# Optimization experiments

Measured on AMD Instinct MI355X. Metric: run time of the kernel, lower is better.

Reference implementation:

```python
import jax, jax.numpy as jnp
import numpy as np

EMBED = 1024

def setup_inputs() -> dict:
    key = jax.random.key(0)
    ks = jax.random.split(key, 7)
    s = 1.0 / np.sqrt(EMBED)
    x = jax.random.normal(ks[0], (8, 2048, EMBED), dtype=jnp.float32)
    Wq = jax.random.normal(ks[1], (EMBED, EMBED), dtype=jnp.float32) * s
    bq = jax.random.normal(ks[2], (EMBED,), dtype=jnp.float32) * s
    Wk = jax.random.normal(ks[3], (EMBED, EMBED), dtype=jnp.float32) * s
    bk = jax.random.normal(ks[4], (EMBED,), dtype=jnp.float32) * s
    Wv = jax.random.normal(ks[5], (EMBED, EMBED), dtype=jnp.float32) * s
    bv = jax.random.normal(ks[6], (EMBED,), dtype=jnp.float32) * s
    return {"x": x, "Wq": Wq, "bq": bq, "Wk": Wk, "bk": bk, "Wv": Wv, "bv": bv}

def reference(x, Wq, bq, Wk, bk, Wv, bv):
    # Linear layers: y = x @ W^T + b (torch convention)
    Q = jnp.einsum('bse,fe->bsf', x, Wq) + bq
    K = jnp.einsum('bse,fe->bsf', x, Wk) + bk
    V = jnp.einsum('bse,fe->bsf', x, Wv) + bv
    scale = 1.0 / jnp.sqrt(jnp.asarray(x.shape[-1], x.dtype))
    scores = jnp.einsum('bqe,bke->bqk', Q, K) * scale  # [B, S, S]
    weights = jax.nn.softmax(scores, axis=-1)
    # dropout is identity in eval mode (deterministic reference)
    return jnp.einsum('bqk,bke->bqe', weights, V)
```

## Files before the change

### kernel.cpp

```cpp
#include <hip/hip_runtime.h>

typedef __bf16 bf16x8 __attribute__((ext_vector_type(8)));
typedef float f32x4 __attribute__((ext_vector_type(4)));

__device__ __forceinline__ unsigned short f2bf(float f) {
  unsigned int u = __builtin_bit_cast(unsigned int, f);
  u += 0x7fffu + ((u >> 16) & 1u);
  return (unsigned short)(u >> 16);
}

__device__ __forceinline__ void async16(const void* g, void* l) {
  __builtin_amdgcn_global_load_lds(
      (const __attribute__((address_space(1))) unsigned int*)g,
      (__attribute__((address_space(3))) unsigned int*)l, 16, 0, 0);
}

#define MFMA(a, b, c) __builtin_amdgcn_mfma_f32_16x16x32_bf16((a), (b), (c), 0, 0, 0)

__global__ __launch_bounds__(256) void pack_bf16(const float* __restrict__ src,
                                                 unsigned short* __restrict__ dst,
                                                 long n) {
  long i = ((long)blockIdx.x * blockDim.x + threadIdx.x) * 4;
  long stride = (long)gridDim.x * blockDim.x * 4;
  for (; i < n; i += stride) {
    float4 v = *(const float4*)(src + i);
    ushort4 o;
    o.x = f2bf(v.x); o.y = f2bf(v.y); o.z = f2bf(v.z); o.w = f2bf(v.w);
    *(ushort4*)(dst + i) = o;
  }
}

template <int EPI>
__global__ __launch_bounds__(512, 1) void gemm256(
    const unsigned short* __restrict__ A, long sAz,
    const unsigned short* __restrict__ B, long sBz,
    int lda, int ldb, int nt,
    float* __restrict__ Cf, long sCz, int ldc, float scale,
    unsigned short* __restrict__ Cq, long sQz, int ldq,
    const float* __restrict__ bq, const float* __restrict__ bk,
    const float* __restrict__ bv,
    float* __restrict__ psum, const float* __restrict__ rsum) {
  extern __shared__ __align__(16) char smem[];
  const int tid = threadIdx.x;
  const int l = tid & 63;
  const int w = tid >> 6;
  const int wm = w >> 2, wn = w & 3;
  int bm = blockIdx.x;
  if ((gridDim.x & 7) == 0) {
    int cpx = gridDim.x >> 3;
    bm = (bm & 7) * cpx + (bm >> 3);
  }
  const int bn = blockIdx.y, bz = blockIdx.z;
  const unsigned short* Ab = A + (long)bz * sAz + (long)bm * 256 * lda;
  const unsigned short* Bb = B + (long)bz * sBz + (long)bn * 256 * ldb;

  const int r0 = tid >> 3;
  const int sch = (tid & 7) ^ (r0 & 7);
  const int l15 = l & 15;
  const int kof = (l >> 4) << 3;

  const int aslot = wm * 16384;
  const int bslot = 32768 + (wn >> 1) * 16384;
  const int brow0 = (wn & 1) * 64;

  int aof[8][2], bof[4][2];
#pragma unroll
  for (int fr = 0; fr < 8; ++fr)
#pragma unroll
    for (int ks = 0; ks < 2; ++ks) {
      int rins = fr * 16 + l15;
      int byte = aslot + rins * 128 + (ks * 32 + kof) * 2;
      aof[fr][ks] = byte ^ ((rins & 7) << 4);
    }
#pragma unroll
  for (int fc = 0; fc < 4; ++fc)
#pragma unroll
    for (int ks = 0; ks < 2; ++ks) {
      int rins = brow0 + fc * 16 + l15;
      int byte = bslot + rins * 128 + (ks * 32 + kof) * 2;
      bof[fc][ks] = byte ^ ((rins & 7) << 4);
    }

  const unsigned short* pa0 = Ab + (long)r0 * lda + sch * 8;
  const unsigned short* pa1 = pa0 + (long)64 * lda;
  const unsigned short* pa2 = pa0 + (long)128 * lda;
  const unsigned short* pa3 = pa0 + (long)192 * lda;
  const unsigned short* pb0 = Bb + (long)r0 * ldb + sch * 8;
  const unsigned short* pb1 = pb0 + (long)64 * ldb;
  const unsigned short* pb2 = pb0 + (long)128 * ldb;
  const unsigned short* pb3 = pb0 + (long)192 * ldb;

  char* sdst = smem + (tid << 4);

  f32x4 acc[8][4] = {};
  bf16x8 bfr[4][2];

#define LDA_FRAG(dst, bb, fr, ks) \
  dst = *(const bf16x8*)(smem + (aof[fr][ks] + (bb)));
#define LDB_FRAG(dst, bb, fc, ks) \
  dst = *(const bf16x8*)(smem + (bof[fc][ks] + (bb)));

  async16(pb0, sdst + 32768);         async16(pb1, sdst + 40960);
  async16(pb2, sdst + 49152);         async16(pb3, sdst + 57344);
  async16(pa0, sdst + 0);             async16(pa1, sdst + 8192);
  async16(pa2, sdst + 16384);         async16(pa3, sdst + 24576);
  async16(pb0 + 64, sdst + 98304);    async16(pb1 + 64, sdst + 106496);
  async16(pb2 + 64, sdst + 114688);   async16(pb3 + 64, sdst + 122880);
  asm volatile("s_waitcnt vmcnt(4)" ::: "memory");
  __builtin_amdgcn_s_barrier();
  pa0 += 64; pa1 += 64; pa2 += 64; pa3 += 64;
  pb0 += 128; pb1 += 128; pb2 += 128; pb3 += 128;

  for (int t = 0; t < nt; ++t) {
    const int buf = (t & 1) << 16;
    const int nbuf = buf ^ 65536;

    bf16x8 a00, a01, a10, a11;

    LDA_FRAG(a00, buf, 0, 0); LDA_FRAG(a01, buf, 0, 1);
    LDA_FRAG(a10, buf, 1, 0); LDA_FRAG(a11, buf, 1, 1);
#pragma unroll
    for (int fc = 0; fc < 4; ++fc) {
      LDB_FRAG(bfr[fc][0], buf, fc, 0);
      LDB_FRAG(bfr[fc][1], buf, fc, 1);
    }
    async16(pa0, sdst + nbuf);
    async16(pa1, sdst + nbuf + 8192);
    __builtin_amdgcn_s_barrier();
    __builtin_amdgcn_s_setprio(1);
#pragma unroll
    for (int fc = 0; fc < 4; ++fc) {
      acc[0][fc] = MFMA(a00, bfr[fc][0], acc[0][fc]);
      acc[0][fc] = MFMA(a01, bfr[fc][1], acc[0][fc]);
      acc[1][fc] = MFMA(a10, bfr[fc][0], acc[1][fc]);
      acc[1][fc] = MFMA(a11, bfr[fc][1], acc[1][fc]);
    }
    __builtin_amdgcn_s_setprio(0);
    __builtin_amdgcn_s_barrier();

    LDA_FRAG(a00, buf, 2, 0); LDA_FRAG(a01, buf, 2, 1);
    LDA_FRAG(a10, buf, 3, 0); LDA_FRAG(a11, buf, 3, 1);
    async16(pa2, sdst + nbuf + 16384);
    async16(pa3, sdst + nbuf + 24576);
    __builtin_amdgcn_s_barrier();
    __builtin_amdgcn_s_setprio(1);
#pragma unroll
    for (int fc = 0; fc < 4; ++fc) {
      acc[2][fc] = MFMA(a00, bfr[fc][0], acc[2][fc]);
      acc[2][fc] = MFMA(a01, bfr[fc][1], acc[2][fc]);
      acc[3][fc] = MFMA(a10, bfr[fc][0], acc[3][fc]);
      acc[3][fc] = MFMA(a11, bfr[fc][1], acc[3][fc]);
    }
    __builtin_amdgcn_s_setprio(0);
    __builtin_amdgcn_s_barrier();

    LDA_FRAG(a00, buf, 4, 0); LDA_FRAG(a01, buf, 4, 1);
    LDA_FRAG(a10, buf, 5, 0); LDA_FRAG(a11, buf, 5, 1);
    async16(pb0, sdst + buf + 32768);
    async16(pb1, sdst + buf + 40960);
    __builtin_amdgcn_s_barrier();
    __builtin_amdgcn_s_setprio(1);
#pragma unroll
    for (int fc = 0; fc < 4; ++fc) {
      acc[4][fc] = MFMA(a00, bfr[fc][0], acc[4][fc]);
      acc[4][fc] = MFMA(a01, bfr[fc][1], acc[4][fc]);
      acc[5][fc] = MFMA(a10, bfr[fc][0], acc[5][fc]);
      acc[5][fc] = MFMA(a11, bfr[fc][1], acc[5][fc]);
    }
    __builtin_amdgcn_s_setprio(0);
    __builtin_amdgcn_s_barrier();

    LDA_FRAG(a00, buf, 6, 0); LDA_FRAG(a01, buf, 6, 1);
    LDA_FRAG(a10, buf, 7, 0); LDA_FRAG(a11, buf, 7, 1);
    async16(pb2, sdst + buf + 49152);
    async16(pb3, sdst + buf + 57344);
    __builtin_amdgcn_s_barrier();
    __builtin_amdgcn_s_setprio(1);
#pragma unroll
    for (int fc = 0; fc < 4; ++fc) {
      acc[6][fc] = MFMA(a00, bfr[fc][0], acc[6][fc]);
      acc[6][fc] = MFMA(a01, bfr[fc][1], acc[6][fc]);
      acc[7][fc] = MFMA(a10, bfr[fc][0], acc[7][fc]);
      acc[7][fc] = MFMA(a11, bfr[fc][1], acc[7][fc]);
    }
    __builtin_amdgcn_s_setprio(0);
    asm volatile("s_waitcnt vmcnt(4)" ::: "memory");
    __builtin_amdgcn_s_barrier();

    if (t < nt - 2) { pa0 += 64; pa1 += 64; pa2 += 64; pa3 += 64; }
    if (t < nt - 3) { pb0 += 64; pb1 += 64; pb2 += 64; pb3 += 64; }
  }

  asm volatile("s_waitcnt vmcnt(0)" ::: "memory");
  __builtin_amdgcn_s_barrier();

  const int rl = (l >> 4) * 4;

  if constexpr (EPI == 0) {
    const int which = (bn * 256) >> 10;
    const int colbase = bn * 256 + wn * 64;
    const float* bias = (which == 0) ? bq : (which == 1) ? bk : bv;
    if (which < 2) {
#pragma unroll
      for (int fr = 0; fr < 8; ++fr)
#pragma unroll
        for (int fc = 0; fc < 4; ++fc) {
          int lc = fc * 16 + l15;
          float bv_ = bias[(colbase + lc) & 1023];
#pragma unroll
          for (int rr = 0; rr < 4; ++rr) {
            int lr = fr * 16 + rl + rr;
            int byte = w * 16384 + lr * 128 + lc * 2;
            byte ^= (lr & 7) << 4;
            *(unsigned short*)(smem + byte) = f2bf(acc[fr][fc][rr] + bv_);
          }
        }
      __syncthreads();
      const long brow = (long)bm * 256;
      const int cw0 = (bn * 256) & 1023;
#pragma unroll
      for (int it = 0; it < 16; ++it) {
        int f = it * 512 + tid;
        int r = f >> 5, ch = f & 31;
        int wv = (r >> 7) * 4 + (ch >> 3);
        int byte = wv * 16384 + (r & 127) * 128 + (ch & 7) * 16;
        byte ^= (r & 7) << 4;
        uint4 val = *(const uint4*)(smem + byte);
        unsigned short* d = Cq + (long)which * 16777216L +
                            (brow + r) * 1024 + cw0 + ch * 8;
        *(uint4*)d = val;
      }
    } else {
#pragma unroll
      for (int fr = 0; fr < 8; ++fr)
#pragma unroll
        for (int fc = 0; fc < 4; ++fc) {
          int lc = wn * 64 + fc * 16 + l15;
          float bv_ = bias[(colbase + fc * 16 + l15) & 1023];
#pragma unroll
          for (int rr = 0; rr < 4; ++rr) {
            int r = wm * 128 + fr * 16 + rl + rr;
            int byte = lc * 512 + r * 2;
            byte ^= (lc & 7) << 4;
            *(unsigned short*)(smem + byte) = f2bf(acc[fr][fc][rr] + bv_);
          }
        }
      __syncthreads();
      const long brow = (long)bm * 256;
      const long b = brow >> 11;
      const long s0 = brow & 2047;
      unsigned short* VT = Cq + 2L * 16777216;
#pragma unroll
      for (int it = 0; it < 16; ++it) {
        int f = it * 512 + tid;
        int c = f >> 5, ch = f & 31;
        int byte = (c * 512 + ch * 16) ^ ((c & 7) << 4);
        uint4 val = *(const uint4*)(smem + byte);
        int d = (bn * 256 - 2048) + c;
        unsigned short* dst = VT + b * 2097152 + (long)d * 2048 + s0 + ch * 8;
        *(uint4*)dst = val;
      }
    }
  } else if constexpr (EPI == 3) {
    float rs[4];
#pragma unroll
    for (int fr = 0; fr < 8; ++fr) {
      rs[0] = rs[1] = rs[2] = rs[3] = 0.0f;
#pragma unroll
      for (int fc = 0; fc < 4; ++fc) {
        int lc = fc * 16 + l15;
#pragma unroll
        for (int rr = 0; rr < 4; ++rr) {
          float e = __expf(acc[fr][fc][rr] * scale);
          rs[rr] += e;
          int lr = fr * 16 + rl + rr;
          int byte = w * 16384 + lr * 128 + lc * 2;
          byte ^= (lr & 7) << 4;
          *(unsigned short*)(smem + byte) = f2bf(e);
        }
      }
#pragma unroll
      for (int rr = 0; rr < 4; ++rr) {
        float v = rs[rr];
#pragma unroll
        for (int o = 1; o < 16; o <<= 1) v += __shfl_xor(v, o);
        if (l15 == 0) {
          int row = wm * 128 + fr * 16 + rl + rr;
          *(float*)(smem + 131072 + (wn * 256 + row) * 4) = v;
        }
      }
    }
    __syncthreads();
    const long brow = (long)bm * 256;
#pragma unroll
    for (int it = 0; it < 16; ++it) {
      int f = it * 512 + tid;
      int r = f >> 5, ch = f & 31;
      int wv = (r >> 7) * 4 + (ch >> 3);
      int byte = wv * 16384 + (r & 127) * 128 + (ch & 7) * 16;
      byte ^= (r & 7) << 4;
      uint4 val = *(const uint4*)(smem + byte);
      unsigned short* d = Cq + (long)bz * sQz + (brow + r) * ldq + bn * 256 + ch * 8;
      *(uint4*)d = val;
    }
    if (tid < 256) {
      float s4 = *(const float*)(smem + 131072 + tid * 4) +
                 *(const float*)(smem + 131072 + 1024 + tid * 4) +
                 *(const float*)(smem + 131072 + 2048 + tid * 4) +
                 *(const float*)(smem + 131072 + 3072 + tid * 4);
      psum[(((long)bz * 2048) + brow + tid) * 8 + bn] = s4;
    }
  } else {
    float* C = Cf + (long)bz * sCz;
    const float* rsb = rsum + (long)bz * 2048;
    const long grbase = (long)bm * 256 + wm * 128;
    const int gcbase = bn * 256 + wn * 64;
#pragma unroll
    for (int fr = 0; fr < 8; ++fr)
#pragma unroll
      for (int rr = 0; rr < 4; ++rr) {
        long gr = grbase + fr * 16 + rl + rr;
        float inv = rsb[gr];
#pragma unroll
        for (int fc = 0; fc < 4; ++fc)
          C[gr * ldc + gcbase + fc * 16 + l15] = acc[fr][fc][rr] * inv;
      }
  }
#undef LDA_FRAG
#undef LDB_FRAG
}

__global__ __launch_bounds__(256) void reduce_psum(const float* __restrict__ p,
                                                   float* __restrict__ r, int n) {
  int i = blockIdx.x * 256 + threadIdx.x;
  if (i < n) {
    const float* q = p + (long)i * 8;
    float s = q[0] + q[1] + q[2] + q[3] + q[4] + q[5] + q[6] + q[7];
    r[i] = 1.0f / s;
  }
}

__global__ void sentinel_kernel(float* out, float v) { out[0] = v; }

extern "C" void kernel_launch(void* const* d_in, const int* in_sizes, int n_in,
                              void* d_out, int out_size, void* d_ws, size_t ws_size,
                              hipStream_t stream) {
  const float* x  = (const float*)d_in[0];
  const float* Wq = (const float*)d_in[1];
  const float* bq = (const float*)d_in[2];
  const float* Wk = (const float*)d_in[3];
  const float* bk = (const float*)d_in[4];
  const float* Wv = (const float*)d_in[5];
  const float* bv = (const float*)d_in[6];
  float* out = (float*)d_out;

  (void)hipFuncSetAttribute((const void*)gemm256<0>,
      hipFuncAttributeMaxDynamicSharedMemorySize, 135168);
  (void)hipFuncSetAttribute((const void*)gemm256<3>,
      hipFuncAttributeMaxDynamicSharedMemorySize, 135168);
  (void)hipFuncSetAttribute((const void*)gemm256<4>,
      hipFuncAttributeMaxDynamicSharedMemorySize, 135168);

  const size_t NEED_BIG2 = 208207872;
  const size_t NEED_SM2  = 140509184;
  if (ws_size < NEED_SM2) {
    sentinel_kernel<<<1, 1, 0, stream>>>(out, (float)ws_size);
    return;
  }
  const bool big = (ws_size >= NEED_BIG2);
  char* ws = (char*)d_ws;
  unsigned short* qkv = (unsigned short*)(ws);
  unsigned short* xb  = (unsigned short*)(ws + 100663296);
  unsigned short* wb  = (unsigned short*)(ws + 134217728);
  unsigned short* wt  = big ? (unsigned short*)(ws + 140509184)
                            : (unsigned short*)(ws + 100663296);
  float* psum = big ? (float*)(ws + 207618048) : (float*)(ws + 117440512);
  float* rsum = big ? (float*)(ws + 208142336) : (float*)(ws + 117571584);

  const float scale = 0.03125f;

  pack_bf16<<<dim3(4096), dim3(256), 0, stream>>>(x, xb, 16777216L);
  pack_bf16<<<dim3(1024), dim3(256), 0, stream>>>(Wq, wb, 1048576L);
  pack_bf16<<<dim3(1024), dim3(256), 0, stream>>>(Wk, wb + 1048576, 1048576L);
  pack_bf16<<<dim3(1024), dim3(256), 0, stream>>>(Wv, wb + 2097152, 1048576L);

  gemm256<0><<<dim3(64, 12, 1), dim3(512), 135168, stream>>>(
      xb, 0L, wb, 0L, 1024, 1024, 16,
      nullptr, 0L, 0, 1.0f, qkv, 0L, 1024, bq, bk, bv, nullptr, nullptr);

  const int bpp = big ? 8 : 2;
  const int npasses = 8 / bpp;
  for (int p = 0; p < npasses; ++p) {
    long b0 = (long)p * bpp;
    long boff = b0 * 2048 * 1024;
    gemm256<3><<<dim3(8, 8, bpp), dim3(512), 135168, stream>>>(
        qkv + boff, 2048L * 1024, qkv + 16777216 + boff, 2048L * 1024,
        1024, 1024, 16,
        nullptr, 0L, 0, scale, wt, 2048L * 2048, 2048,
        nullptr, nullptr, nullptr, psum, nullptr);

    reduce_psum<<<dim3(8 * bpp), dim3(256), 0, stream>>>(psum, rsum, 2048 * bpp);

    gemm256<4><<<dim3(8, 4, bpp), dim3(512), 135168, stream>>>(
        wt, 2048L * 2048, qkv + 2L * 16777216 + b0 * 2097152, 2097152L,
        2048, 2048, 32,
        out + boff, 2048L * 1024, 1024, 1.0f, nullptr, 0L, 0,
        nullptr, nullptr, nullptr, nullptr, rsum);
  }
}
```

Measured before the change: 288.5 us.

## Software-pipeline A-fragment LDS loads, drop intra-iteration barriers, fuse psum reduction

The GEMM main loop now double-buffers A fragments in registers (c/n sets), loading the next group while MFMAs on the current group run. It removes most of the per-quarter barriers so that only one mid-loop and one end-of-iteration barrier remain. LDS offsets are computed from base cores plus constants instead of per-fragment arrays, which cuts register use. Separately, the three weight pack launches become one kernel, and the reduce_psum kernel is removed by computing the row reciprocal in the PV epilogue. Dropping barriers risks races on the LDS buffers being overwritten by async loads, and the epilogue now reads eight partial sums per row redundantly.

```diff
diff --git a/kernel.cpp b/kernel.cpp
--- a/kernel.cpp
+++ b/kernel.cpp
@@ -30,6 +30,18 @@
   }
 }
 
+__global__ __launch_bounds__(256) void pack_w3(const float* __restrict__ s0,
+                                               const float* __restrict__ s1,
+                                               const float* __restrict__ s2,
+                                               unsigned short* __restrict__ dst) {
+  const float* s = (blockIdx.y == 0) ? s0 : (blockIdx.y == 1) ? s1 : s2;
+  long i = ((long)blockIdx.x * 256 + threadIdx.x) * 4;
+  float4 v = *(const float4*)(s + i);
+  ushort4 o;
+  o.x = f2bf(v.x); o.y = f2bf(v.y); o.z = f2bf(v.z); o.w = f2bf(v.w);
+  *(ushort4*)(dst + (long)blockIdx.y * 1048576 + i) = o;
+}
+
 template <int EPI>
 __global__ __launch_bounds__(512, 1) void gemm256(
     const unsigned short* __restrict__ A, long sAz,
@@ -38,8 +50,7 @@
     float* __restrict__ Cf, long sCz, int ldc, float scale,
     unsigned short* __restrict__ Cq, long sQz, int ldq,
     const float* __restrict__ bq, const float* __restrict__ bk,
-    const float* __restrict__ bv,
-    float* __restrict__ psum, const float* __restrict__ rsum) {
+    const float* __restrict__ bv, float* __restrict__ psum) {
   extern __shared__ __align__(16) char smem[];
   const int tid = threadIdx.x;
   const int l = tid & 63;
@@ -63,23 +74,11 @@
   const int bslot = 32768 + (wn >> 1) * 16384;
   const int brow0 = (wn & 1) * 64;
 
-  int aof[8][2], bof[4][2];
-#pragma unroll
-  for (int fr = 0; fr < 8; ++fr)
-#pragma unroll
-    for (int ks = 0; ks < 2; ++ks) {
-      int rins = fr * 16 + l15;
-      int byte = aslot + rins * 128 + (ks * 32 + kof) * 2;
-      aof[fr][ks] = byte ^ ((rins & 7) << 4);
-    }
-#pragma unroll
-  for (int fc = 0; fc < 4; ++fc)
-#pragma unroll
-    for (int ks = 0; ks < 2; ++ks) {
-      int rins = brow0 + fc * 16 + l15;
-      int byte = bslot + rins * 128 + (ks * 32 + kof) * 2;
-      bof[fc][ks] = byte ^ ((rins & 7) << 4);
-    }
+  const int amask = (l15 & 7) << 4;
+  const int acore0 = (aslot + l15 * 128 + kof * 2) ^ amask;
+  const int acore1 = (aslot + l15 * 128 + 64 + kof * 2) ^ amask;
+  const int bcore0 = (bslot + (brow0 + l15) * 128 + kof * 2) ^ amask;
+  const int bcore1 = (bslot + (brow0 + l15) * 128 + 64 + kof * 2) ^ amask;
 
   const unsigned short* pa0 = Ab + (long)r0 * lda + sch * 8;
   const unsigned short* pa1 = pa0 + (long)64 * lda;
@@ -94,11 +93,13 @@
 
   f32x4 acc[8][4] = {};
   bf16x8 bfr[4][2];
-
-#define LDA_FRAG(dst, bb, fr, ks) \
-  dst = *(const bf16x8*)(smem + (aof[fr][ks] + (bb)));
-#define LDB_FRAG(dst, bb, fc, ks) \
-  dst = *(const bf16x8*)(smem + (bof[fc][ks] + (bb)));
+  bf16x8 c00, c01, c10, c11;
+  bf16x8 n00, n01, n10, n11;
+
+#define LDA_F(dst, bb, fr, ks) \
+  dst = *(const bf16x8*)(smem + (((ks) ? acore1 : acore0) + (fr)*2048 + (bb)));
+#define LDB_F(dst, bb, fc, ks) \
+  dst = *(const bf16x8*)(smem + (((ks) ? bcore1 : bcore0) + (fc)*2048 + (bb)));
 
   async16(pb0, sdst + 32768);         async16(pb1, sdst + 40960);
   async16(pb2, sdst + 49152);         async16(pb3, sdst + 57344);
@@ -111,81 +112,77 @@
   pa0 += 64; pa1 += 64; pa2 += 64; pa3 += 64;
   pb0 += 128; pb1 += 128; pb2 += 128; pb3 += 128;
 
+  LDA_F(c00, 0, 0, 0); LDA_F(c01, 0, 0, 1);
+  LDA_F(c10, 0, 1, 0); LDA_F(c11, 0, 1, 1);
+
   for (int t = 0; t < nt; ++t) {
     const int buf = (t & 1) << 16;
     const int nbuf = buf ^ 65536;
 
-    bf16x8 a00, a01, a10, a11;
-
-    LDA_FRAG(a00, buf, 0, 0); LDA_FRAG(a01, buf, 0, 1);
-    LDA_FRAG(a10, buf, 1, 0); LDA_FRAG(a11, buf, 1, 1);
-#pragma unroll
-    for (int fc = 0; fc < 4; ++fc) {
-      LDB_FRAG(bfr[fc][0], buf, fc, 0);
-      LDB_FRAG(bfr[fc][1], buf, fc, 1);
-    }
+#pragma unroll
+    for (int fc = 0; fc < 4; ++fc) {
+      LDB_F(bfr[fc][0], buf, fc, 0);
+      LDB_F(bfr[fc][1], buf, fc, 1);
+    }
+    LDA_F(n00, buf, 2, 0); LDA_F(n01, buf, 2, 1);
+    LDA_F(n10, buf, 3, 0); LDA_F(n11, buf, 3, 1);
     async16(pa0, sdst + nbuf);
     async16(pa1, sdst + nbuf + 8192);
-    __builtin_amdgcn_s_barrier();
     __builtin_amdgcn_s_setprio(1);
 #pragma unroll
     for (int fc = 0; fc < 4; ++fc) {
-      acc[0][fc] = MFMA(a00, bfr[fc][0], acc[0][fc]);
-      acc[0][fc] = MFMA(a01, bfr[fc][1], acc[0][fc]);
-      acc[1][fc] = MFMA(a10, bfr[fc][0], acc[1][fc]);
-      acc[1][fc] = MFMA(a11, bfr[fc][1], acc[1][fc]);
+      acc[0][fc] = MFMA(c00, bfr[fc][0], acc[0][fc]);
+      acc[0][fc] = MFMA(c01, bfr[fc][1], acc[0][fc]);
+      acc[1][fc] = MFMA(c10, bfr[fc][0], acc[1][fc]);
+      acc[1][fc] = MFMA(c11, bfr[fc][1], acc[1][fc]);
+    }
+    __builtin_amdgcn_s_setprio(0);
+
+    LDA_F(c00, buf, 4, 0); LDA_F(c01, buf, 4, 1);
+    LDA_F(c10, buf, 5, 0); LDA_F(c11, buf, 5, 1);
+    async16(pa2, sdst + nbuf + 16384);
+    async16(pa3, sdst + nbuf + 24576);
+    __builtin_amdgcn_s_setprio(1);
+#pragma unroll
+    for (int fc = 0; fc < 4; ++fc) {
+      acc[2][fc] = MFMA(n00, bfr[fc][0], acc[2][fc]);
+      acc[2][fc] = MFMA(n01, bfr[fc][1], acc[2][fc]);
+      acc[3][fc] = MFMA(n10, bfr[fc][0], acc[3][fc]);
+      acc[3][fc] = MFMA(n11, bfr[fc][1], acc[3][fc]);
     }
     __builtin_amdgcn_s_setprio(0);
     __builtin_amdgcn_s_barrier();
 
-    LDA_FRAG(a00, buf, 2, 0); LDA_FRAG(a01, buf, 2, 1);
-    LDA_FRAG(a10, buf, 3, 0); LDA_FRAG(a11, buf, 3, 1);
-    async16(pa2, sdst + nbuf + 16384);
-    async16(pa3, sdst + nbuf + 24576);
-    __builtin_amdgcn_s_barrier();
-    __builtin_amdgcn_s_setprio(1);
-#pragma unroll
-    for (int fc = 0; fc < 4; ++fc) {
-      acc[2][fc] = MFMA(a00, bfr[fc][0], acc[2][fc]);
-      acc[2][fc] = MFMA(a01, bfr[fc][1], acc[2][fc]);
-      acc[3][fc] = MFMA(a10, bfr[fc][0], acc[3][fc]);
-      acc[3][fc] = MFMA(a11, bfr[fc][1], acc[3][fc]);
-    }
-    __builtin_amdgcn_s_setprio(0);
-    __builtin_amdgcn_s_barrier();
-
-    LDA_FRAG(a00, buf, 4, 0); LDA_FRAG(a01, buf, 4, 1);
-    LDA_FRAG(a10, buf, 5, 0); LDA_FRAG(a11, buf, 5, 1);
+    LDA_F(n00, buf, 6, 0); LDA_F(n01, buf, 6, 1);
+    LDA_F(n10, buf, 7, 0); LDA_F(n11, buf, 7, 1);
     async16(pb0, sdst + buf + 32768);
     async16(pb1, sdst + buf + 40960);
-    __builtin_amdgcn_s_barrier();
     __builtin_amdgcn_s_setprio(1);
 #pragma unroll
     for (int fc = 0; fc < 4; ++fc) {
-      acc[4][fc] = MFMA(a00, bfr[fc][0], acc[4][fc]);
-      acc[4][fc] = MFMA(a01, bfr[fc][1], acc[4][fc]);
-      acc[5][fc] = MFMA(a10, bfr[fc][0], acc[5][fc]);
-      acc[5][fc] = MFMA(a11, bfr[fc][1], acc[5][fc]);
+      acc[4][fc] = MFMA(c00, bfr[fc][0], acc[4][fc]);
+      acc[4][fc] = MFMA(c01, bfr[fc][1], acc[4][fc]);
+      acc[5][fc] = MFMA(c10, bfr[fc][0], acc[5][fc]);
+      acc[5][fc] = MFMA(c11, bfr[fc][1], acc[5][fc]);
     }
     __builtin_amdgcn_s_setprio(0);
-    __builtin_amdgcn_s_barrier();
-
-    LDA_FRAG(a00, buf, 6, 0); LDA_FRAG(a01, buf, 6, 1);
-    LDA_FRAG(a10, buf, 7, 0); LDA_FRAG(a11, buf, 7, 1);
+
     async16(pb2, sdst + buf + 49152);
     async16(pb3, sdst + buf + 57344);
-    __builtin_amdgcn_s_barrier();
     __builtin_amdgcn_s_setprio(1);
 #pragma unroll
     for (int fc = 0; fc < 4; ++fc) {
-      acc[6][fc] = MFMA(a00, bfr[fc][0], acc[6][fc]);
-      acc[6][fc] = MFMA(a01, bfr[fc][1], acc[6][fc]);
-      acc[7][fc] = MFMA(a10, bfr[fc][0], acc[7][fc]);
-      acc[7][fc] = MFMA(a11, bfr[fc][1], acc[7][fc]);
+      acc[6][fc] = MFMA(n00, bfr[fc][0], acc[6][fc]);
+      acc[6][fc] = MFMA(n01, bfr[fc][1], acc[6][fc]);
+      acc[7][fc] = MFMA(n10, bfr[fc][0], acc[7][fc]);
+      acc[7][fc] = MFMA(n11, bfr[fc][1], acc[7][fc]);
     }
     __builtin_amdgcn_s_setprio(0);
     asm volatile("s_waitcnt vmcnt(4)" ::: "memory");
     __builtin_amdgcn_s_barrier();
+
+    LDA_F(c00, nbuf, 0, 0); LDA_F(c01, nbuf, 0, 1);
+    LDA_F(c10, nbuf, 1, 0); LDA_F(c11, nbuf, 1, 1);
 
     if (t < nt - 2) { pa0 += 64; pa1 += 64; pa2 += 64; pa3 += 64; }
     if (t < nt - 3) { pb0 += 64; pb1 += 64; pb2 += 64; pb3 += 64; }
@@ -312,7 +309,6 @@
     }
   } else {
     float* C = Cf + (long)bz * sCz;
-    const float* rsb = rsum + (long)bz * 2048;
     const long grbase = (long)bm * 256 + wm * 128;
     const int gcbase = bn * 256 + wn * 64;
 #pragma unroll
@@ -320,24 +316,18 @@
 #pragma unroll
       for (int rr = 0; rr < 4; ++rr) {
         long gr = grbase + fr * 16 + rl + rr;
-        float inv = rsb[gr];
+        const float* pp = psum + (((long)bz * 2048) + gr) * 8;
+        float4 s0 = *(const float4*)pp;
+        float4 s1 = *(const float4*)(pp + 4);
+        float inv = 1.0f / (s0.x + s0.y + s0.z + s0.w +
+                            s1.x + s1.y + s1.z + s1.w);
 #pragma unroll
         for (int fc = 0; fc < 4; ++fc)
           C[gr * ldc + gcbase + fc * 16 + l15] = acc[fr][fc][rr] * inv;
       }
   }
-#undef LDA_FRAG
-#undef LDB_FRAG
-}
-
-__global__ __launch_bounds__(256) void reduce_psum(const float* __restrict__ p,
-                                                   float* __restrict__ r, int n) {
-  int i = blockIdx.x * 256 + threadIdx.x;
-  if (i < n) {
-    const float* q = p + (long)i * 8;
-    float s = q[0] + q[1] + q[2] + q[3] + q[4] + q[5] + q[6] + q[7];
-    r[i] = 1.0f / s;
-  }
+#undef LDA_F
+#undef LDB_F
 }
 
 __global__ void sentinel_kernel(float* out, float v) { out[0] = v; }
@@ -375,18 +365,15 @@
   unsigned short* wt  = big ? (unsigned short*)(ws + 140509184)
                             : (unsigned short*)(ws + 100663296);
   float* psum = big ? (float*)(ws + 207618048) : (float*)(ws + 117440512);
-  float* rsum = big ? (float*)(ws + 208142336) : (float*)(ws + 117571584);
 
   const float scale = 0.03125f;
 
   pack_bf16<<<dim3(4096), dim3(256), 0, stream>>>(x, xb, 16777216L);
-  pack_bf16<<<dim3(1024), dim3(256), 0, stream>>>(Wq, wb, 1048576L);
-  pack_bf16<<<dim3(1024), dim3(256), 0, stream>>>(Wk, wb + 1048576, 1048576L);
-  pack_bf16<<<dim3(1024), dim3(256), 0, stream>>>(Wv, wb + 2097152, 1048576L);
+  pack_w3<<<dim3(1024, 3), dim3(256), 0, stream>>>(Wq, Wk, Wv, wb);
 
   gemm256<0><<<dim3(64, 12, 1), dim3(512), 135168, stream>>>(
       xb, 0L, wb, 0L, 1024, 1024, 16,
-      nullptr, 0L, 0, 1.0f, qkv, 0L, 1024, bq, bk, bv, nullptr, nullptr);
+      nullptr, 0L, 0, 1.0f, qkv, 0L, 1024, bq, bk, bv, nullptr);
 
   const int bpp = big ? 8 : 2;
   const int npasses = 8 / bpp;
@@ -397,14 +384,12 @@
         qkv + boff, 2048L * 1024, qkv + 16777216 + boff, 2048L * 1024,
         1024, 1024, 16,
         nullptr, 0L, 0, scale, wt, 2048L * 2048, 2048,
-        nullptr, nullptr, nullptr, psum, nullptr);
-
-    reduce_psum<<<dim3(8 * bpp), dim3(256), 0, stream>>>(psum, rsum, 2048 * bpp);
+        nullptr, nullptr, nullptr, psum);
 
     gemm256<4><<<dim3(8, 4, bpp), dim3(512), 135168, stream>>>(
         wt, 2048L * 2048, qkv + 2L * 16777216 + b0 * 2097152, 2097152L,
         2048, 2048, 32,
         out + boff, 2048L * 1024, 1024, 1.0f, nullptr, 0L, 0,
-        nullptr, nullptr, nullptr, nullptr, rsum);
-  }
-}
+        nullptr, nullptr, nullptr, psum);
+  }
+}
```

Measured after the change: 269.0 us, median of 2. 6.7% less time.
